# Optimization experiments

Measured on AMD Instinct MI355X. Metric: run time of the kernel, lower is better.

The kernel has to match this reference:

```python
import jax, jax.numpy as jnp
import numpy as np

B, S, D, H, L = 32, 512, 1024, 1024, 2
SCALE = 1.0 / np.sqrt(H)  # keep activations sane


def setup_inputs() -> dict:
    key = jax.random.key(0)
    ks = jax.random.split(key, 9)
    return {
        "x":   jax.random.normal(ks[0], (B, S, D), dtype=jnp.float32),
        "Wx0": jax.random.normal(ks[1], (4 * H, D), dtype=jnp.float32) * SCALE,
        "Wh0": jax.random.normal(ks[2], (4 * H, H), dtype=jnp.float32) * SCALE,
        "bx0": jax.random.normal(ks[3], (4 * H,), dtype=jnp.float32) * SCALE,
        "bh0": jax.random.normal(ks[4], (4 * H,), dtype=jnp.float32) * SCALE,
        "Wx1": jax.random.normal(ks[5], (4 * H, H), dtype=jnp.float32) * SCALE,
        "Wh1": jax.random.normal(ks[6], (4 * H, H), dtype=jnp.float32) * SCALE,
        "bx1": jax.random.normal(ks[7], (4 * H,), dtype=jnp.float32) * SCALE,
        "bh1": jax.random.normal(ks[8], (4 * H,), dtype=jnp.float32) * SCALE,
    }


def reference(x, Wx0, Wh0, bx0, bh0, Wx1, Wh1, bx1, bh1):
    Wx, Wh, bx, bh = [Wx0, Wx1], [Wh0, Wh1], [bx0, bx1], [bh0, bh1]

    def step(carry, x_t):
        h, c = carry                      # each [L, B, H]
        inp = x_t                         # [B, D]
        hs, cs = [], []
        for l in range(L):
            gates = inp @ Wx[l].T + bx[l] + h[l] @ Wh[l].T + bh[l]  # [B, 4H]
            f, i, g, o = jnp.split(gates, 4, axis=1)  # torch chunk order: f,i,g,o
            c_new = jax.nn.sigmoid(f) * c[l] + jax.nn.sigmoid(i) * jnp.tanh(g)
            h_new = jax.nn.sigmoid(o) * jnp.tanh(c_new)  # proj is Identity
            hs.append(h_new)
            cs.append(c_new)
            inp = h_new  # dropout p=0 -> identity
        return (jnp.stack(hs), jnp.stack(cs)), hs[-1]

    h0 = jnp.zeros((L, B, H), dtype=x.dtype)
    c0 = jnp.zeros((L, B, H), dtype=x.dtype)
    (h_n, c_n), outs = jax.lax.scan(step, (h0, c0), jnp.transpose(x, (1, 0, 2)))
    outputs = jnp.transpose(outs, (1, 0, 2))  # [B, S, H] (batch_first)
    return outputs, (h_n, c_n)
```

## Files before the change

kernel.cpp:

```cpp
#include <hip/hip_runtime.h>
#include <math.h>

#define Bsz 32
#define Ssz 512
#define Hsz 1024
#define SLOTS 16

typedef _Float16 f16x8 __attribute__((ext_vector_type(8)));
typedef float    f32x4 __attribute__((ext_vector_type(4)));
typedef float    f32x8 __attribute__((ext_vector_type(8)));

struct P {
  const float *x, *Wx0, *Wh0, *bx0, *bh0, *Wx1, *Wh1, *bx1, *bh1;
  unsigned short *h0r;
  unsigned short *h1r;
  unsigned *f0, *f1;
  _Float16 *wsw;
  float *out;
};

__global__ __launch_bounds__(256) void preconv(P p) {
  unsigned idx   = blockIdx.x * 256 + threadIdx.x;
  unsigned lane  = idx & 63;
  unsigned m     = (idx >> 6) & 3;
  unsigned ks    = (idx >> 8) & 63;
  unsigned blk   = (idx >> 14) & 63;
  unsigned layer = idx >> 20;
  unsigned hidx  = blk * 16 + (lane & 15);
  unsigned k     = ks * 32 + (lane >> 4) * 8;
  unsigned row   = m * 1024 + hidx;
  const float* src;
  if (layer == 0) src = (k < 1024) ? p.Wx0 + (size_t)row * 1024 + k
                                   : p.Wh0 + (size_t)row * 1024 + (k - 1024);
  else            src = (k < 1024) ? p.Wx1 + (size_t)row * 1024 + k
                                   : p.Wh1 + (size_t)row * 1024 + (k - 1024);
  f32x8 v = __builtin_nontemporal_load(reinterpret_cast<const f32x8*>(src));
  f16x8 h;
#pragma unroll
  for (int j = 0; j < 8; ++j) h[j] = (_Float16)v[j];
  *reinterpret_cast<f16x8*>(p.wsw + (size_t)idx * 8) = h;
}

__device__ inline void load_xfrag(const float* xp, f16x8& Bh, f16x8& Bl) {
  f32x8 v = *reinterpret_cast<const f32x8*>(xp);
#pragma unroll
  for (int j = 0; j < 8; ++j) {
    _Float16 hv = (_Float16)v[j];
    Bh[j] = hv; Bl[j] = (_Float16)(v[j] - (float)hv);
  }
}

__global__ __launch_bounds__(512, 2) void lstm_persist(P p) {
  const int blk   = blockIdx.x;
  const int layer = blk >> 6;
  const int hb    = blk & 63;
  const int tid   = threadIdx.x;
  const int w     = tid >> 6;
  const int lane  = tid & 63;
  const int nl    = lane & 15;
  const int quad  = lane >> 4;

  __shared__ float red[8][64 * 33];
  __shared__ float csl[Bsz * 16];
  __shared__ float bsum[64];

  if (tid < 64) {
    int r = (tid >> 4) * 1024 + hb * 16 + (tid & 15);
    bsum[tid] = layer ? (p.bx1[r] + p.bh1[r]) : (p.bx0[r] + p.bh0[r]);
  }
  csl[tid] = 0.f;
  __syncthreads();

  const _Float16* wslab = p.wsw + (size_t)(layer * 64 + hb) * 131072;
  f16x8 Wr[32];
#pragma unroll
  for (int kk = 0; kk < 8; ++kk)
#pragma unroll
    for (int m = 0; m < 4; ++m)
      Wr[kk * 4 + m] = *reinterpret_cast<const f16x8*>(
          wslab + (size_t)(((w * 8 + kk) * 4 + m) * 64 + lane) * 8);

  const bool xwave = (layer == 0) && (w < 4);
  const int  kloc  = (w & 3) * 256;

  for (int s = 0; s < Ssz; ++s) {
    if (layer == 0) {
      if (xwave) {
        if (s >= 16) {
          const unsigned* fp = p.f1 + (s & 15) * 64 + lane;
          unsigned need = (unsigned)(s - 15);
          while (__hip_atomic_load(fp, __ATOMIC_RELAXED, __HIP_MEMORY_SCOPE_AGENT) < need)
            __builtin_amdgcn_s_sleep(2);
        }
      } else if (s >= 1) {
        const unsigned* fp = p.f0 + ((s - 1) & 15) * 64 + (w & 3) * 16 + nl;
        unsigned need = (unsigned)s;
        while (__hip_atomic_load(fp, __ATOMIC_RELAXED, __HIP_MEMORY_SCOPE_AGENT) < need)
          __builtin_amdgcn_s_sleep(2);
      }
    } else {
      if (w < 4) {
        const unsigned* fp = p.f0 + (s & 15) * 64 + (w & 3) * 16 + nl;
        unsigned need = (unsigned)(s + 1);
        while (__hip_atomic_load(fp, __ATOMIC_RELAXED, __HIP_MEMORY_SCOPE_AGENT) < need)
          __builtin_amdgcn_s_sleep(2);
      } else if (s >= 1) {
        const unsigned* fp = p.f1 + ((s - 1) & 15) * 64 + (w & 3) * 16 + nl;
        unsigned need = (unsigned)s;
        while (__hip_atomic_load(fp, __ATOMIC_RELAXED, __HIP_MEMORY_SCOPE_AGENT) < need)
          __builtin_amdgcn_s_sleep(2);
      }
    }

    if (!xwave && ((s & 7) == 0))
      __builtin_amdgcn_fence(__ATOMIC_ACQUIRE, "agent");

    f32x4 acc[4][2];
#pragma unroll
    for (int m = 0; m < 4; ++m)
#pragma unroll
      for (int nt = 0; nt < 2; ++nt) acc[m][nt] = (f32x4){0.f, 0.f, 0.f, 0.f};

    if (xwave) {
      const float* xbase = p.x + (size_t)s * 1024 + kloc;
      f16x8 Bh[2][2], Bl[2][2];
      load_xfrag(xbase + (size_t)nl        * (Ssz * 1024) + quad * 8, Bh[0][0], Bl[0][0]);
      load_xfrag(xbase + (size_t)(nl + 16) * (Ssz * 1024) + quad * 8, Bh[0][1], Bl[0][1]);
#pragma unroll
      for (int kk = 0; kk < 8; ++kk) {
        const int cur = kk & 1, nxt = cur ^ 1;
        if (kk < 7) {
          const int ko = (kk + 1) * 32 + quad * 8;
          load_xfrag(xbase + (size_t)nl        * (Ssz * 1024) + ko, Bh[nxt][0], Bl[nxt][0]);
          load_xfrag(xbase + (size_t)(nl + 16) * (Ssz * 1024) + ko, Bh[nxt][1], Bl[nxt][1]);
        }
#pragma unroll
        for (int m = 0; m < 4; ++m) {
          f16x8 A = Wr[kk * 4 + m];
#pragma unroll
          for (int nt = 0; nt < 2; ++nt) {
            acc[m][nt] = __builtin_amdgcn_mfma_f32_16x16x32_f16(A, Bh[cur][nt], acc[m][nt], 0, 0, 0);
            acc[m][nt] = __builtin_amdgcn_mfma_f32_16x16x32_f16(A, Bl[cur][nt], acc[m][nt], 0, 0, 0);
          }
        }
      }
    } else {
      const unsigned short* rbase;
      if (layer == 0) rbase = p.h0r + ((s - 1) & 15) * 65536;
      else if (w < 4) rbase = p.h0r + (s & 15) * 65536;
      else            rbase = p.h1r + ((s - 1) & 15) * 65536;
      const _Float16* fb = (const _Float16*)rbase + ((w & 3) * 32 + quad) * 512 + nl * 16;
#pragma unroll
      for (int kk = 0; kk < 8; ++kk) {
        const _Float16* fp2 = fb + kk * 2048;
        f16x8 Bh0 = *reinterpret_cast<const f16x8*>(fp2);
        f16x8 Bl0 = *reinterpret_cast<const f16x8*>(fp2 + 8);
        f16x8 Bh1 = *reinterpret_cast<const f16x8*>(fp2 + 256);
        f16x8 Bl1 = *reinterpret_cast<const f16x8*>(fp2 + 264);
#pragma unroll
        for (int m = 0; m < 4; ++m) {
          f16x8 A = Wr[kk * 4 + m];
          acc[m][0] = __builtin_amdgcn_mfma_f32_16x16x32_f16(A, Bh0, acc[m][0], 0, 0, 0);
          acc[m][0] = __builtin_amdgcn_mfma_f32_16x16x32_f16(A, Bl0, acc[m][0], 0, 0, 0);
          acc[m][1] = __builtin_amdgcn_mfma_f32_16x16x32_f16(A, Bh1, acc[m][1], 0, 0, 0);
          acc[m][1] = __builtin_amdgcn_mfma_f32_16x16x32_f16(A, Bl1, acc[m][1], 0, 0, 0);
        }
      }
    }

#pragma unroll
    for (int m = 0; m < 4; ++m)
#pragma unroll
      for (int nt = 0; nt < 2; ++nt)
#pragma unroll
        for (int r = 0; r < 4; ++r)
          red[w][(m * 16 + quad * 4 + r) * 33 + nt * 16 + nl] = acc[m][nt][r];
    __syncthreads();
#pragma unroll
    for (int j = 0; j < 4; ++j) {
      int idx = tid + j * 512;
      int ad = (idx >> 5) * 33 + (idx & 31);
      float ssum = red[0][ad] + red[1][ad] + red[2][ad] + red[3][ad]
                 + red[4][ad] + red[5][ad] + red[6][ad] + red[7][ad];
      red[0][ad] = ssum;
    }
    __syncthreads();

    {
      int hl = tid & 15, b = tid >> 4;
      float gf = red[0][(0 * 16 + hl) * 33 + b] + bsum[0 * 16 + hl];
      float gi = red[0][(1 * 16 + hl) * 33 + b] + bsum[1 * 16 + hl];
      float gg = red[0][(2 * 16 + hl) * 33 + b] + bsum[2 * 16 + hl];
      float go = red[0][(3 * 16 + hl) * 33 + b] + bsum[3 * 16 + hl];
      float f  = 1.f / (1.f + __expf(-gf));
      float i  = 1.f / (1.f + __expf(-gi));
      float g  = tanhf(gg);
      float o  = 1.f / (1.f + __expf(-go));
      float c  = f * csl[b * 16 + hl] + i * g;
      float hn = o * tanhf(c);
      csl[b * 16 + hl] = c;
      _Float16 hh  = (_Float16)hn;
      _Float16 hlo = (_Float16)(hn - (float)hh);
      unsigned short hbits = __builtin_bit_cast(unsigned short, hh);
      unsigned short lbits = __builtin_bit_cast(unsigned short, hlo);
      int hg   = hb * 16 + hl;
      int koct = hb * 2 + (hl >> 3), jj = hl & 7;
      int fragoff = koct * 512 + b * 16 + jj;
      if (layer == 0) {
        unsigned short* dst = p.h0r + (s & 15) * 65536 + fragoff;
        __hip_atomic_store(dst,     hbits, __ATOMIC_RELAXED, __HIP_MEMORY_SCOPE_AGENT);
        __hip_atomic_store(dst + 8, lbits, __ATOMIC_RELAXED, __HIP_MEMORY_SCOPE_AGENT);
      } else {
        unsigned short* dst = p.h1r + (s & 15) * 65536 + fragoff;
        __hip_atomic_store(dst,     hbits, __ATOMIC_RELAXED, __HIP_MEMORY_SCOPE_AGENT);
        __hip_atomic_store(dst + 8, lbits, __ATOMIC_RELAXED, __HIP_MEMORY_SCOPE_AGENT);
        __builtin_nontemporal_store(hn, p.out + (size_t)b * (Ssz * Hsz) + (size_t)s * Hsz + hg);
      }
      if (s == Ssz - 1) {
        float* tail = p.out + (size_t)Bsz * Ssz * Hsz;
        __builtin_nontemporal_store(hn, tail + layer * 32768 + b * 1024 + hg);
        __builtin_nontemporal_store(c,  tail + 65536 + layer * 32768 + b * 1024 + hg);
      }
    }
    __syncthreads();
    if (tid == 0) {
      if (layer == 0)
        __hip_atomic_store(p.f0 + (s & 15) * 64 + hb, (unsigned)(s + 1),
                           __ATOMIC_RELAXED, __HIP_MEMORY_SCOPE_AGENT);
      else
        __hip_atomic_store(p.f1 + (s & 15) * 64 + hb, (unsigned)(s + 1),
                           __ATOMIC_RELAXED, __HIP_MEMORY_SCOPE_AGENT);
    }
  }
}

extern "C" void kernel_launch(void* const* d_in, const int* in_sizes, int n_in,
                              void* d_out, int out_size, void* d_ws, size_t ws_size,
                              hipStream_t stream) {
  char* ws = (char*)d_ws;
  P p;
  p.x   = (const float*)d_in[0];
  p.Wx0 = (const float*)d_in[1]; p.Wh0 = (const float*)d_in[2];
  p.bx0 = (const float*)d_in[3]; p.bh0 = (const float*)d_in[4];
  p.Wx1 = (const float*)d_in[5]; p.Wh1 = (const float*)d_in[6];
  p.bx1 = (const float*)d_in[7]; p.bh1 = (const float*)d_in[8];

  p.h0r = (unsigned short*)(ws);
  p.h1r = (unsigned short*)(ws + 2097152);
  p.f0  = (unsigned*)(ws + 4194304);
  p.f1  = (unsigned*)(ws + 4198400);
  p.wsw = (_Float16*)(ws + 8388608);
  p.out = (float*)d_out;

  hipMemsetAsync(d_ws, 0, 4202496, stream);
  preconv<<<dim3(8192), dim3(256), 0, stream>>>(p);
  lstm_persist<<<dim3(128), dim3(512), 0, stream>>>(p);
}
```

Before: 7.334 ms.

## Replace per-step flag polling with tagged h-ring data validation and retry

Removes the per-step spin on producer flags before reading the hidden-state ring. Each stored fp16 hi/lo half now carries step-parity tag bits in spare exponent bits. Consumers issue coherent loads, check the tags, retry until every lane sees fresh data, then strip the tags before the MFMAs. Flags are kept only for ring-slot reuse back-pressure (13 slots), the ring is pre-seeded with invalid tags in preconv, and the full barriers become LDS-only waits. The risk is correctness: stealing exponent bits only works when the values stay small enough, and the retry loads add latency and memory traffic.

```diff
diff --git a/kernel.cpp b/kernel.cpp
--- a/kernel.cpp
+++ b/kernel.cpp
@@ -4,7 +4,7 @@
 #define Bsz 32
 #define Ssz 512
 #define Hsz 1024
-#define SLOTS 16
+#define SLOTS 13
 
 typedef _Float16 f16x8 __attribute__((ext_vector_type(8)));
 typedef float    f32x4 __attribute__((ext_vector_type(4)));
@@ -20,7 +20,11 @@
 };
 
 __global__ __launch_bounds__(256) void preconv(P p) {
-  unsigned idx   = blockIdx.x * 256 + threadIdx.x;
+  unsigned idx = blockIdx.x * 256 + threadIdx.x;
+  if (idx < 851968u) {
+    if (idx < 425984u) ((unsigned*)p.h0r)[idx] = 0x70003000u;
+    else               ((unsigned*)p.h1r)[idx - 425984u] = 0x70003000u;
+  }
   unsigned lane  = idx & 63;
   unsigned m     = (idx >> 6) & 3;
   unsigned ks    = (idx >> 8) & 63;
@@ -50,6 +54,50 @@
   }
 }
 
+union U16x8 { f32x4 f; unsigned u[4]; f16x8 h; };
+
+__device__ inline unsigned chk2(f32x4 hf, f32x4 lf, unsigned pp, unsigned tt) {
+  U16x8 H, L; H.f = hf; L.f = lf;
+  unsigned x = ((H.u[0]^pp)|(H.u[1]^pp)|(H.u[2]^pp)|(H.u[3]^pp)) & 0x40004000u;
+  unsigned y = ((L.u[0]^tt)|(L.u[1]^tt)|(L.u[2]^tt)|(L.u[3]^tt)) & 0x70007000u;
+  return x | y;
+}
+__device__ inline f16x8 strip_hi(f32x4 v) {
+  U16x8 X; X.f = v;
+  X.u[0]&=0xBFFFBFFFu; X.u[1]&=0xBFFFBFFFu; X.u[2]&=0xBFFFBFFFu; X.u[3]&=0xBFFFBFFFu;
+  return X.h;
+}
+__device__ inline f16x8 strip_lo(f32x4 v) {
+  U16x8 X; X.f = v;
+  X.u[0]&=0x8FFF8FFFu; X.u[1]&=0x8FFF8FFFu; X.u[2]&=0x8FFF8FFFu; X.u[3]&=0x8FFF8FFFu;
+  return X.h;
+}
+
+__device__ inline void issue_group(unsigned long long sb, unsigned voff,
+    f32x4& a0, f32x4& a1, f32x4& a2, f32x4& a3,
+    f32x4& a4, f32x4& a5, f32x4& a6, f32x4& a7) {
+  asm volatile(
+    "global_load_dwordx4 %0, %8, %9 offset:-2048 sc0 sc1\n\t"
+    "global_load_dwordx4 %1, %8, %9 offset:-2032 sc0 sc1\n\t"
+    "global_load_dwordx4 %2, %8, %9 offset:-1536 sc0 sc1\n\t"
+    "global_load_dwordx4 %3, %8, %9 offset:-1520 sc0 sc1\n\t"
+    "global_load_dwordx4 %4, %8, %9 offset:2048 sc0 sc1\n\t"
+    "global_load_dwordx4 %5, %8, %9 offset:2064 sc0 sc1\n\t"
+    "global_load_dwordx4 %6, %8, %9 offset:2560 sc0 sc1\n\t"
+    "global_load_dwordx4 %7, %8, %9 offset:2576 sc0 sc1"
+    : "=&v"(a0), "=&v"(a1), "=&v"(a2), "=&v"(a3),
+      "=&v"(a4), "=&v"(a5), "=&v"(a6), "=&v"(a7)
+    : "v"(voff), "s"(sb));
+}
+
+#define WAITV(N) do { asm volatile("s_waitcnt vmcnt(" #N ")" ::: "memory"); \
+                      __builtin_amdgcn_sched_barrier(0); } while (0)
+
+__device__ inline void bar_lds() {
+  asm volatile("s_waitcnt lgkmcnt(0)" ::: "memory");
+  __builtin_amdgcn_s_barrier();
+}
+
 __global__ __launch_bounds__(512, 2) void lstm_persist(P p) {
   const int blk   = blockIdx.x;
   const int layer = blk >> 6;
@@ -84,37 +132,6 @@
   const int  kloc  = (w & 3) * 256;
 
   for (int s = 0; s < Ssz; ++s) {
-    if (layer == 0) {
-      if (xwave) {
-        if (s >= 16) {
-          const unsigned* fp = p.f1 + (s & 15) * 64 + lane;
-          unsigned need = (unsigned)(s - 15);
-          while (__hip_atomic_load(fp, __ATOMIC_RELAXED, __HIP_MEMORY_SCOPE_AGENT) < need)
-            __builtin_amdgcn_s_sleep(2);
-        }
-      } else if (s >= 1) {
-        const unsigned* fp = p.f0 + ((s - 1) & 15) * 64 + (w & 3) * 16 + nl;
-        unsigned need = (unsigned)s;
-        while (__hip_atomic_load(fp, __ATOMIC_RELAXED, __HIP_MEMORY_SCOPE_AGENT) < need)
-          __builtin_amdgcn_s_sleep(2);
-      }
-    } else {
-      if (w < 4) {
-        const unsigned* fp = p.f0 + (s & 15) * 64 + (w & 3) * 16 + nl;
-        unsigned need = (unsigned)(s + 1);
-        while (__hip_atomic_load(fp, __ATOMIC_RELAXED, __HIP_MEMORY_SCOPE_AGENT) < need)
-          __builtin_amdgcn_s_sleep(2);
-      } else if (s >= 1) {
-        const unsigned* fp = p.f1 + ((s - 1) & 15) * 64 + (w & 3) * 16 + nl;
-        unsigned need = (unsigned)s;
-        while (__hip_atomic_load(fp, __ATOMIC_RELAXED, __HIP_MEMORY_SCOPE_AGENT) < need)
-          __builtin_amdgcn_s_sleep(2);
-      }
-    }
-
-    if (!xwave && ((s & 7) == 0))
-      __builtin_amdgcn_fence(__ATOMIC_ACQUIRE, "agent");
-
     f32x4 acc[4][2];
 #pragma unroll
     for (int m = 0; m < 4; ++m)
@@ -145,26 +162,74 @@
         }
       }
     } else {
-      const unsigned short* rbase;
-      if (layer == 0) rbase = p.h0r + ((s - 1) & 15) * 65536;
-      else if (w < 4) rbase = p.h0r + (s & 15) * 65536;
-      else            rbase = p.h1r + ((s - 1) & 15) * 65536;
-      const _Float16* fb = (const _Float16*)rbase + ((w & 3) * 32 + quad) * 512 + nl * 16;
-#pragma unroll
-      for (int kk = 0; kk < 8; ++kk) {
-        const _Float16* fp2 = fb + kk * 2048;
-        f16x8 Bh0 = *reinterpret_cast<const f16x8*>(fp2);
-        f16x8 Bl0 = *reinterpret_cast<const f16x8*>(fp2 + 8);
-        f16x8 Bh1 = *reinterpret_cast<const f16x8*>(fp2 + 256);
-        f16x8 Bl1 = *reinterpret_cast<const f16x8*>(fp2 + 264);
-#pragma unroll
-        for (int m = 0; m < 4; ++m) {
-          f16x8 A = Wr[kk * 4 + m];
-          acc[m][0] = __builtin_amdgcn_mfma_f32_16x16x32_f16(A, Bh0, acc[m][0], 0, 0, 0);
-          acc[m][0] = __builtin_amdgcn_mfma_f32_16x16x32_f16(A, Bl0, acc[m][0], 0, 0, 0);
-          acc[m][1] = __builtin_amdgcn_mfma_f32_16x16x32_f16(A, Bh1, acc[m][1], 0, 0, 0);
-          acc[m][1] = __builtin_amdgcn_mfma_f32_16x16x32_f16(A, Bl1, acc[m][1], 0, 0, 0);
-        }
+      int t; const unsigned short* ringp;
+      if (layer == 0)    { t = s - 1; ringp = p.h0r; }
+      else if (w < 4)    { t = s;     ringp = p.h0r; }
+      else               { t = s - 1; ringp = p.h1r; }
+      if (t >= 0) {
+        unsigned slot = (unsigned)t % SLOTS;
+        unsigned pp = (unsigned)((t & 1) << 14); pp |= pp << 16;
+        unsigned tt = (unsigned)((t & 7) << 12); tt |= tt << 16;
+        unsigned long long sbv = (unsigned long long)(uintptr_t)ringp
+            + (unsigned long long)slot * 131072u + (unsigned)(w & 3) * 32768u + 2048u;
+        unsigned sblo = __builtin_amdgcn_readfirstlane((unsigned)sbv);
+        unsigned sbhi = __builtin_amdgcn_readfirstlane((unsigned)(sbv >> 32));
+        unsigned long long sb = ((unsigned long long)sbhi << 32) | sblo;
+        unsigned voff = (unsigned)(quad * 1024 + nl * 32);
+
+        f32x4 A0,A1,A2,A3,A4,A5,A6,A7, B0,B1,B2,B3,B4,B5,B6,B7;
+#define CHKA (chk2(A0,A1,pp,tt)|chk2(A2,A3,pp,tt)|chk2(A4,A5,pp,tt)|chk2(A6,A7,pp,tt))
+#define CHKB (chk2(B0,B1,pp,tt)|chk2(B2,B3,pp,tt)|chk2(B4,B5,pp,tt)|chk2(B6,B7,pp,tt))
+#define RETRYA(OFF) do { unsigned bad_ = CHKA; \
+      while (__any((int)(bad_ != 0u))) { \
+        issue_group(sb + (OFF), voff, A0,A1,A2,A3,A4,A5,A6,A7); WAITV(0); bad_ = CHKA; } } while (0)
+#define RETRYB(OFF) do { unsigned bad_ = CHKB; \
+      while (__any((int)(bad_ != 0u))) { \
+        issue_group(sb + (OFF), voff, B0,B1,B2,B3,B4,B5,B6,B7); WAITV(0); bad_ = CHKB; } } while (0)
+#define DO_KK(KK, Xh0, Xl0, Xh1, Xl1) do { \
+      f16x8 bh0_ = strip_hi(Xh0), bl0_ = strip_lo(Xl0); \
+      f16x8 bh1_ = strip_hi(Xh1), bl1_ = strip_lo(Xl1); \
+      _Pragma("unroll") \
+      for (int m_ = 0; m_ < 4; ++m_) { \
+        f16x8 Aw_ = Wr[(KK) * 4 + m_]; \
+        acc[m_][0] = __builtin_amdgcn_mfma_f32_16x16x32_f16(Aw_, bh0_, acc[m_][0], 0, 0, 0); \
+        acc[m_][0] = __builtin_amdgcn_mfma_f32_16x16x32_f16(Aw_, bl0_, acc[m_][0], 0, 0, 0); \
+        acc[m_][1] = __builtin_amdgcn_mfma_f32_16x16x32_f16(Aw_, bh1_, acc[m_][1], 0, 0, 0); \
+        acc[m_][1] = __builtin_amdgcn_mfma_f32_16x16x32_f16(Aw_, bl1_, acc[m_][1], 0, 0, 0); \
+      } } while (0)
+
+        issue_group(sb,         voff, A0,A1,A2,A3,A4,A5,A6,A7);
+        issue_group(sb + 8192,  voff, B0,B1,B2,B3,B4,B5,B6,B7);
+        WAITV(8);  RETRYA(0);
+        DO_KK(0, A0,A1,A2,A3); DO_KK(1, A4,A5,A6,A7);
+        issue_group(sb + 16384, voff, A0,A1,A2,A3,A4,A5,A6,A7);
+        WAITV(8);  RETRYB(8192);
+        DO_KK(2, B0,B1,B2,B3); DO_KK(3, B4,B5,B6,B7);
+        issue_group(sb + 24576, voff, B0,B1,B2,B3,B4,B5,B6,B7);
+        WAITV(8);  RETRYA(16384);
+        DO_KK(4, A0,A1,A2,A3); DO_KK(5, A4,A5,A6,A7);
+        WAITV(0);  RETRYB(24576);
+        DO_KK(6, B0,B1,B2,B3); DO_KK(7, B4,B5,B6,B7);
+#undef CHKA
+#undef CHKB
+#undef RETRYA
+#undef RETRYB
+#undef DO_KK
+      }
+    }
+
+    if (s >= SLOTS) {
+      if (layer == 0) {
+        const unsigned* a = p.f0 + ((unsigned)(s - 12) % SLOTS) * 64 + lane;
+        while (__hip_atomic_load(a, __ATOMIC_RELAXED, __HIP_MEMORY_SCOPE_AGENT) < (unsigned)(s - 11))
+          __builtin_amdgcn_s_sleep(2);
+        const unsigned* b = p.f1 + ((unsigned)(s - 13) % SLOTS) * 64 + lane;
+        while (__hip_atomic_load(b, __ATOMIC_RELAXED, __HIP_MEMORY_SCOPE_AGENT) < (unsigned)(s - 12))
+          __builtin_amdgcn_s_sleep(2);
+      } else {
+        const unsigned* a = p.f1 + ((unsigned)(s - 12) % SLOTS) * 64 + lane;
+        while (__hip_atomic_load(a, __ATOMIC_RELAXED, __HIP_MEMORY_SCOPE_AGENT) < (unsigned)(s - 11))
+          __builtin_amdgcn_s_sleep(2);
       }
     }
 
@@ -175,7 +240,7 @@
 #pragma unroll
         for (int r = 0; r < 4; ++r)
           red[w][(m * 16 + quad * 4 + r) * 33 + nt * 16 + nl] = acc[m][nt][r];
-    __syncthreads();
+    bar_lds();
 #pragma unroll
     for (int j = 0; j < 4; ++j) {
       int idx = tid + j * 512;
@@ -184,7 +249,7 @@
                  + red[4][ad] + red[5][ad] + red[6][ad] + red[7][ad];
       red[0][ad] = ssum;
     }
-    __syncthreads();
+    bar_lds();
 
     {
       int hl = tid & 15, b = tid >> 4;
@@ -201,17 +266,20 @@
       csl[b * 16 + hl] = c;
       _Float16 hh  = (_Float16)hn;
       _Float16 hlo = (_Float16)(hn - (float)hh);
-      unsigned short hbits = __builtin_bit_cast(unsigned short, hh);
-      unsigned short lbits = __builtin_bit_cast(unsigned short, hlo);
+      unsigned short hbits = (unsigned short)(__builtin_bit_cast(unsigned short, hh)
+                                              | (unsigned short)((s & 1) << 14));
+      unsigned short lbits = (unsigned short)(__builtin_bit_cast(unsigned short, hlo)
+                                              | (unsigned short)((s & 7) << 12));
       int hg   = hb * 16 + hl;
       int koct = hb * 2 + (hl >> 3), jj = hl & 7;
+      unsigned slot_s = (unsigned)s % SLOTS;
       int fragoff = koct * 512 + b * 16 + jj;
       if (layer == 0) {
-        unsigned short* dst = p.h0r + (s & 15) * 65536 + fragoff;
+        unsigned short* dst = p.h0r + slot_s * 65536 + fragoff;
         __hip_atomic_store(dst,     hbits, __ATOMIC_RELAXED, __HIP_MEMORY_SCOPE_AGENT);
         __hip_atomic_store(dst + 8, lbits, __ATOMIC_RELAXED, __HIP_MEMORY_SCOPE_AGENT);
       } else {
-        unsigned short* dst = p.h1r + (s & 15) * 65536 + fragoff;
+        unsigned short* dst = p.h1r + slot_s * 65536 + fragoff;
         __hip_atomic_store(dst,     hbits, __ATOMIC_RELAXED, __HIP_MEMORY_SCOPE_AGENT);
         __hip_atomic_store(dst + 8, lbits, __ATOMIC_RELAXED, __HIP_MEMORY_SCOPE_AGENT);
         __builtin_nontemporal_store(hn, p.out + (size_t)b * (Ssz * Hsz) + (size_t)s * Hsz + hg);
@@ -222,13 +290,14 @@
         __builtin_nontemporal_store(c,  tail + 65536 + layer * 32768 + b * 1024 + hg);
       }
     }
-    __syncthreads();
+    bar_lds();
     if (tid == 0) {
+      unsigned slot_s = (unsigned)s % SLOTS;
       if (layer == 0)
-        __hip_atomic_store(p.f0 + (s & 15) * 64 + hb, (unsigned)(s + 1),
+        __hip_atomic_store(p.f0 + slot_s * 64 + hb, (unsigned)(s + 1),
                            __ATOMIC_RELAXED, __HIP_MEMORY_SCOPE_AGENT);
       else
-        __hip_atomic_store(p.f1 + (s & 15) * 64 + hb, (unsigned)(s + 1),
+        __hip_atomic_store(p.f1 + slot_s * 64 + hb, (unsigned)(s + 1),
                            __ATOMIC_RELAXED, __HIP_MEMORY_SCOPE_AGENT);
     }
   }
@@ -252,7 +321,7 @@
   p.wsw = (_Float16*)(ws + 8388608);
   p.out = (float*)d_out;
 
-  hipMemsetAsync(d_ws, 0, 4202496, stream);
+  hipMemsetAsync(ws + 4194304, 0, 8192, stream);
   preconv<<<dim3(8192), dim3(256), 0, stream>>>(p);
   lstm_persist<<<dim3(128), dim3(512), 0, stream>>>(p);
 }
```

Measured after the change: 7.934 ms. 8.2% more time.

## Stage h fragments in LDS and publish with vector stores before flag

Applied to the files above, without the earlier changes.

Each block's new hidden-state fragment now goes into a small shared staging buffer first. Two waves then write it to the global ring with 16-byte stores marked sc0 sc1, replacing 1024 scattered 2-byte atomic stores. The ready flag is raised before the non-critical output stores instead of after them, and two LDS barriers use a lighter waitcnt-plus-barrier in place of __syncthreads. This shortens the critical path between steps on the recurrent dependency, but visibility ordering now relies on the inline-asm store cache bits and the barrier. That carries a risk of memory-ordering bugs if the relaxed flag store overtakes the data.

```diff
diff --git a/kernel.cpp b/kernel.cpp
--- a/kernel.cpp
+++ b/kernel.cpp
@@ -50,6 +50,11 @@
   }
 }
 
+__device__ inline void bar_lds() {
+  asm volatile("s_waitcnt lgkmcnt(0)" ::: "memory");
+  __builtin_amdgcn_s_barrier();
+}
+
 __global__ __launch_bounds__(512, 2) void lstm_persist(P p) {
   const int blk   = blockIdx.x;
   const int layer = blk >> 6;
@@ -63,6 +68,7 @@
   __shared__ float red[8][64 * 33];
   __shared__ float csl[Bsz * 16];
   __shared__ float bsum[64];
+  __shared__ unsigned short stage[1024];
 
   if (tid < 64) {
     int r = (tid >> 4) * 1024 + hb * 16 + (tid & 15);
@@ -175,7 +181,7 @@
 #pragma unroll
         for (int r = 0; r < 4; ++r)
           red[w][(m * 16 + quad * 4 + r) * 33 + nt * 16 + nl] = acc[m][nt][r];
-    __syncthreads();
+    bar_lds();
 #pragma unroll
     for (int j = 0; j < 4; ++j) {
       int idx = tid + j * 512;
@@ -184,10 +190,11 @@
                  + red[4][ad] + red[5][ad] + red[6][ad] + red[7][ad];
       red[0][ad] = ssum;
     }
-    __syncthreads();
-
+    bar_lds();
+
+    const int hl = tid & 15, b = tid >> 4;
+    float hn, cv;
     {
-      int hl = tid & 15, b = tid >> 4;
       float gf = red[0][(0 * 16 + hl) * 33 + b] + bsum[0 * 16 + hl];
       float gi = red[0][(1 * 16 + hl) * 33 + b] + bsum[1 * 16 + hl];
       float gg = red[0][(2 * 16 + hl) * 33 + b] + bsum[2 * 16 + hl];
@@ -196,40 +203,47 @@
       float i  = 1.f / (1.f + __expf(-gi));
       float g  = tanhf(gg);
       float o  = 1.f / (1.f + __expf(-go));
-      float c  = f * csl[b * 16 + hl] + i * g;
-      float hn = o * tanhf(c);
-      csl[b * 16 + hl] = c;
+      cv = f * csl[b * 16 + hl] + i * g;
+      hn = o * tanhf(cv);
+      csl[b * 16 + hl] = cv;
       _Float16 hh  = (_Float16)hn;
       _Float16 hlo = (_Float16)(hn - (float)hh);
-      unsigned short hbits = __builtin_bit_cast(unsigned short, hh);
-      unsigned short lbits = __builtin_bit_cast(unsigned short, hlo);
-      int hg   = hb * 16 + hl;
-      int koct = hb * 2 + (hl >> 3), jj = hl & 7;
-      int fragoff = koct * 512 + b * 16 + jj;
-      if (layer == 0) {
-        unsigned short* dst = p.h0r + (s & 15) * 65536 + fragoff;
-        __hip_atomic_store(dst,     hbits, __ATOMIC_RELAXED, __HIP_MEMORY_SCOPE_AGENT);
-        __hip_atomic_store(dst + 8, lbits, __ATOMIC_RELAXED, __HIP_MEMORY_SCOPE_AGENT);
-      } else {
-        unsigned short* dst = p.h1r + (s & 15) * 65536 + fragoff;
-        __hip_atomic_store(dst,     hbits, __ATOMIC_RELAXED, __HIP_MEMORY_SCOPE_AGENT);
-        __hip_atomic_store(dst + 8, lbits, __ATOMIC_RELAXED, __HIP_MEMORY_SCOPE_AGENT);
+      int sidx = (hl >> 3) * 512 + b * 16 + (hl & 7);
+      stage[sidx]     = __builtin_bit_cast(unsigned short, hh);
+      stage[sidx + 8] = __builtin_bit_cast(unsigned short, hlo);
+    }
+    bar_lds();
+
+    {
+      unsigned short* ringb = (layer == 0 ? p.h0r : p.h1r)
+                              + ((unsigned)s & 15) * 65536 + hb * 1024;
+      if (w < 2) {
+        int li = w * 64 + lane;
+        f32x4 d = *reinterpret_cast<const f32x4*>(&stage[li * 8]);
+        unsigned long long dst = (unsigned long long)(uintptr_t)(ringb + li * 8);
+        asm volatile("global_store_dwordx4 %0, %1, off sc0 sc1"
+                     :: "v"(dst), "v"(d) : "memory");
+      }
+    }
+    __syncthreads();
+    if (tid == 0) {
+      if (layer == 0)
+        __hip_atomic_store(p.f0 + ((unsigned)s & 15) * 64 + hb, (unsigned)(s + 1),
+                           __ATOMIC_RELAXED, __HIP_MEMORY_SCOPE_AGENT);
+      else
+        __hip_atomic_store(p.f1 + ((unsigned)s & 15) * 64 + hb, (unsigned)(s + 1),
+                           __ATOMIC_RELAXED, __HIP_MEMORY_SCOPE_AGENT);
+    }
+
+    {
+      int hg = hb * 16 + hl;
+      if (layer == 1)
         __builtin_nontemporal_store(hn, p.out + (size_t)b * (Ssz * Hsz) + (size_t)s * Hsz + hg);
-      }
       if (s == Ssz - 1) {
         float* tail = p.out + (size_t)Bsz * Ssz * Hsz;
         __builtin_nontemporal_store(hn, tail + layer * 32768 + b * 1024 + hg);
-        __builtin_nontemporal_store(c,  tail + 65536 + layer * 32768 + b * 1024 + hg);
-      }
-    }
-    __syncthreads();
-    if (tid == 0) {
-      if (layer == 0)
-        __hip_atomic_store(p.f0 + (s & 15) * 64 + hb, (unsigned)(s + 1),
-                           __ATOMIC_RELAXED, __HIP_MEMORY_SCOPE_AGENT);
-      else
-        __hip_atomic_store(p.f1 + (s & 15) * 64 + hb, (unsigned)(s + 1),
-                           __ATOMIC_RELAXED, __HIP_MEMORY_SCOPE_AGENT);
+        __builtin_nontemporal_store(cv, tail + 65536 + layer * 32768 + b * 1024 + hg);
+      }
     }
   }
 }
```

Result: slower. 7.512 ms (+2.4%).
